# Kernel optimization log

Measured on AMD Instinct MI355X. Metric: run time of the kernel, lower is better.

## Reference

```python
import jax, jax.numpy as jnp
import numpy as np

B, S, D = 2, 2048, 4096
N_HEADS, N_KV_HEADS, HEAD_DIM = 32, 8, 128
Q_DIM = N_HEADS * HEAD_DIM        # 4096
KV_DIM = N_KV_HEADS * HEAD_DIM    # 1024
N_REP = N_HEADS // N_KV_HEADS
ROPE_THETA = 500000.0


def make_freqs_cis(seqlen, head_dim, theta):
    # Interleaved (sin, cos) pairs per rotary frequency, matching the module's
    # einsum/flip RoPE convention: row1 = x0*sin + x1*cos, row0 = x0*cos - x1*sin.
    inv_freq = 1.0 / (theta ** (np.arange(0, head_dim, 2, dtype=np.float32) / head_dim))
    t = np.arange(seqlen, dtype=np.float32)
    ang = np.outer(t, inv_freq)                       # [S, hd/2]
    fc = np.stack([np.sin(ang), np.cos(ang)], axis=-1)  # [S, hd/2, 2]
    return jnp.asarray(fc.reshape(seqlen, head_dim))


def apply_rotary_emb(xq, xk, freqs_cis):
    # xq: [B,S,Hq,hd], xk: [B,S,Hkv,hd], freqs_cis: [S,hd]
    xq_shape, xk_shape = xq.shape, xk.shape
    xq2 = xq.reshape(*xq.shape[:-1], -1, 2)
    xk2 = xk.reshape(*xk.shape[:-1], -1, 2)
    fc = freqs_cis.reshape(freqs_cis.shape[0], 1, -1, 2)   # [S,1,hd/2,2]
    # row_1 = <x, fc>
    xq_row1 = jnp.einsum('bshpi,shpi->bshp', xq2, fc)
    xk_row1 = jnp.einsum('bshpi,shpi->bshp', xk2, fc)
    # flipped fc with negated second component: (f1, -f0)
    fc_flip = jnp.flip(fc, axis=-1) * jnp.array([1.0, -1.0], dtype=fc.dtype)
    xq_row0 = jnp.einsum('bshpi,shpi->bshp', xq2, fc_flip)
    xk_row0 = jnp.einsum('bshpi,shpi->bshp', xk2, fc_flip)
    xq_out = jnp.stack([xq_row0, xq_row1], axis=-1).reshape(xq_shape)
    xk_out = jnp.stack([xk_row0, xk_row1], axis=-1).reshape(xk_shape)
    return xq_out, xk_out


def setup_inputs() -> dict:
    key = jax.random.key(0)
    k1, k2, k3 = jax.random.split(key, 3)
    x = jax.random.normal(k1, (B, S, D), dtype=jnp.float32)
    wqkv = jax.random.normal(k2, (D, Q_DIM + 2 * KV_DIM), dtype=jnp.float32) * 0.02
    wo = jax.random.normal(k3, (Q_DIM, D), dtype=jnp.float32) * 0.02
    freqs_cis = make_freqs_cis(S, HEAD_DIM, ROPE_THETA)
    return {"x": x, "freqs_cis": freqs_cis, "wqkv": wqkv, "wo": wo, "is_causal": 1}


def reference(x, freqs_cis, wqkv, wo, is_causal):
    bsz, seqlen, _ = x.shape
    xqkv = jnp.einsum('bsd,de->bse', x, wqkv)
    xq = xqkv[..., :Q_DIM].reshape(bsz, seqlen, N_HEADS, HEAD_DIM)
    xk = xqkv[..., Q_DIM:Q_DIM + KV_DIM].reshape(bsz, seqlen, N_KV_HEADS, HEAD_DIM)
    xv = xqkv[..., Q_DIM + KV_DIM:].reshape(bsz, seqlen, N_KV_HEADS, HEAD_DIM)
    xq, xk = apply_rotary_emb(xq, xk, freqs_cis)
    # [B,H,S,hd]
    xq = xq.transpose(0, 2, 1, 3)
    xk = jnp.repeat(xk.transpose(0, 2, 1, 3), N_REP, axis=1)
    xv = jnp.repeat(xv.transpose(0, 2, 1, 3), N_REP, axis=1)
    scale = 1.0 / jnp.sqrt(jnp.asarray(HEAD_DIM, dtype=xq.dtype))
    scores = jnp.einsum('bhqd,bhkd->bhqk', xq, xk) * scale
    if is_causal:
        mask = jnp.tril(jnp.ones((seqlen, seqlen), dtype=bool))
        scores = jnp.where(mask, scores, jnp.finfo(scores.dtype).min)
    attn = jax.nn.softmax(scores, axis=-1)
    out = jnp.einsum('bhqk,bhkd->bhqd', attn, xv)
    out = out.transpose(0, 2, 1, 3).reshape(bsz, seqlen, Q_DIM)
    return jnp.einsum('bsd,de->bse', out, wo)
```

## Files before the change

kernel.cpp:

```cpp
#include <hip/hip_runtime.h>
#include <stdint.h>
#include <stddef.h>

#define BB 2
#define SS 2048
#define DD 4096
#define NH 32
#define NKV 8
#define HD 128
#define QDIM 4096
#define KVDIM 1024
#define NQKV 6144
#define QK_SCALE_L2E 0.12751744f

typedef __bf16 bf16;
typedef __bf16 bf16x8 __attribute__((ext_vector_type(8)));
typedef __bf16 bf16x4 __attribute__((ext_vector_type(4)));
typedef float f32x4 __attribute__((ext_vector_type(4)));

#define MFMA16(a, b, c) __builtin_amdgcn_mfma_f32_16x16x32_bf16((a), (b), (c), 0, 0, 0)

typedef __attribute__((address_space(1))) void GASV;
typedef __attribute__((address_space(3))) void LASV;

__device__ __forceinline__ void gload_lds16(const void* g, void* l) {
    __builtin_amdgcn_global_load_lds((GASV*)g, (LASV*)l, 16, 0, 0);
}

__device__ __forceinline__ float fexp2(float x) {
    float r;
    asm("v_exp_f32 %0, %1" : "=v"(r) : "v"(x));
    return r;
}

__global__ __launch_bounds__(256) void k_cvt_x(const float* __restrict__ in,
                                               bf16* __restrict__ out) {
    size_t i = ((size_t)blockIdx.x * 256 + threadIdx.x) * 8;
    const float4 a = *(const float4*)(in + i);
    const float4 b = *(const float4*)(in + i + 4);
    bf16x8 v;
    v[0] = (bf16)a.x; v[1] = (bf16)a.y; v[2] = (bf16)a.z; v[3] = (bf16)a.w;
    v[4] = (bf16)b.x; v[5] = (bf16)b.y; v[6] = (bf16)b.z; v[7] = (bf16)b.w;
    *(bf16x8*)(out + i) = v;
}

__global__ __launch_bounds__(256) void k_tr_cvt(const float* __restrict__ in,
                                                bf16* __restrict__ out, int R, int C) {
    __shared__ float tile[64][65];
    const int t = threadIdx.x;
    const int tx = t & 15, ty = t >> 4;
    const int r0 = blockIdx.y * 64, c0 = blockIdx.x * 64;
#pragma unroll
    for (int p = 0; p < 4; ++p) {
        const float4 v = *(const float4*)(in + (size_t)(r0 + p * 16 + ty) * C + c0 + tx * 4);
        tile[p * 16 + ty][tx * 4 + 0] = v.x;
        tile[p * 16 + ty][tx * 4 + 1] = v.y;
        tile[p * 16 + ty][tx * 4 + 2] = v.z;
        tile[p * 16 + ty][tx * 4 + 3] = v.w;
    }
    __syncthreads();
#pragma unroll
    for (int p = 0; p < 4; ++p) {
        const int oc = c0 + p * 16 + ty;
        bf16x4 pk;
#pragma unroll
        for (int j = 0; j < 4; ++j) pk[j] = (bf16)tile[tx * 4 + j][p * 16 + ty];
        *(bf16x4*)(out + (size_t)oc * R + r0 + tx * 4) = pk;
    }
}

__device__ __forceinline__ void stage_tile64(bf16* lds, const bf16* gbase, int ld, int kt) {
    const int tid = threadIdx.x;
    const int lane = tid & 63;
    const int w = tid >> 6;
#pragma unroll
    for (int i = 0; i < 4; ++i) {
        const int phys = i * 4096 + w * 1024 + lane * 16;
        const int row = phys >> 7;
        const int cc = (phys >> 4) & 7;
        const int lc = cc ^ (row & 7);
        gload_lds16(gbase + (size_t)row * ld + kt + lc * 8,
                    (char*)lds + (i * 4096 + w * 1024));
    }
}

__device__ __forceinline__ void gemm_main(const bf16* __restrict__ Atile,
                                          const bf16* __restrict__ Btile,
                                          bf16* As, bf16* Bs, f32x4 acc[4][4]) {
    const int tid = threadIdx.x, lane = tid & 63, w = tid >> 6;
    const int wm = (w >> 1) * 64, wn = (w & 1) * 64;
    const int l15 = lane & 15, l4 = lane >> 4;
    const f32x4 vz = {0.f, 0.f, 0.f, 0.f};
#pragma unroll
    for (int m = 0; m < 4; ++m)
#pragma unroll
        for (int n = 0; n < 4; ++n) acc[m][n] = vz;

    for (int kt = 0; kt < 4096; kt += 64) {
        __syncthreads();
        stage_tile64(As, Atile, 4096, kt);
        stage_tile64(Bs, Btile, 4096, kt);
        __syncthreads();
#pragma unroll
        for (int kc = 0; kc < 2; ++kc) {
            bf16x8 af[4], bfr[4];
#pragma unroll
            for (int m = 0; m < 4; ++m) {
                const int row = wm + m * 16 + l15;
                const int cc = kc * 4 + l4;
                af[m] = *(const bf16x8*)((const char*)As + (row << 7) + ((cc ^ (row & 7)) << 4));
            }
#pragma unroll
            for (int n = 0; n < 4; ++n) {
                const int row = wn + n * 16 + l15;
                const int cc = kc * 4 + l4;
                bfr[n] = *(const bf16x8*)((const char*)Bs + (row << 7) + ((cc ^ (row & 7)) << 4));
            }
#pragma unroll
            for (int m = 0; m < 4; ++m)
#pragma unroll
                for (int n = 0; n < 4; ++n) acc[m][n] = MFMA16(af[m], bfr[n], acc[m][n]);
        }
    }
}

__global__ __launch_bounds__(256) void k_gemm_qkv(const bf16* __restrict__ A,
                                                  const bf16* __restrict__ Bt,
                                                  const float* __restrict__ fc,
                                                  bf16* __restrict__ Qb,
                                                  bf16* __restrict__ Kb,
                                                  bf16* __restrict__ VTb) {
    __shared__ __align__(16) bf16 As[128 * 64];
    __shared__ __align__(16) bf16 Bs[128 * 64];
    f32x4 acc[4][4];
    const int bx = blockIdx.x, by = blockIdx.y;
    gemm_main(A + (size_t)by * 128 * 4096, Bt + (size_t)bx * 128 * 4096, As, Bs, acc);

    const int tid = threadIdx.x, lane = tid & 63, w = tid >> 6;
    const int wm = (w >> 1) * 64, wn = (w & 1) * 64, l15 = lane & 15, l4 = lane >> 4;
    const int n0 = bx * 128 + wn;
#pragma unroll
    for (int m = 0; m < 4; ++m) {
        const int rowbase = by * 128 + wm + m * 16 + l4 * 4;
#pragma unroll
        for (int n = 0; n < 4; ++n) {
            const int col = n0 + n * 16 + l15;
            f32x4 v = acc[m][n];
            if (n0 < QDIM + KVDIM) {
                const int d = col & (HD - 1);
                const int dp = d & ~1;
                const float sgn = (d & 1) ? 1.f : -1.f;
#pragma unroll
                for (int r = 0; r < 4; ++r) {
                    const int row = rowbase + r;
                    const int s = row & (SS - 1);
                    const float2 sc = *(const float2*)(fc + s * HD + dp);
                    const float partner = __shfl_xor(v[r], 1);
                    float res = v[r] * sc.y + sgn * partner * sc.x;
                    if (n0 < QDIM) {
                        res *= QK_SCALE_L2E;
                        Qb[(size_t)row * QDIM + col] = (bf16)res;
                    } else {
                        Kb[(size_t)row * KVDIM + (col - QDIM)] = (bf16)res;
                    }
                }
            } else {
                const int hdv = col - (QDIM + KVDIM);
                const int kvh = hdv >> 7, dd = hdv & (HD - 1);
                const int bb = rowbase >> 11, s = rowbase & (SS - 1);
                bf16x4 pk;
#pragma unroll
                for (int r = 0; r < 4; ++r) pk[r] = (bf16)v[r];
                *(bf16x4*)(VTb + ((size_t)((bb * NKV + kvh) * HD + dd)) * SS + s) = pk;
            }
        }
    }
}

__global__ __launch_bounds__(256, 2) void k_attn(const bf16* __restrict__ Qb,
                                                 const bf16* __restrict__ Kb,
                                                 const bf16* __restrict__ VTb,
                                                 bf16* __restrict__ Ob) {
    __shared__ __align__(16) bf16 Ks[64 * 128];
    __shared__ __align__(16) bf16 Vs[128 * 64];
    __shared__ __align__(16) bf16 Ps[4][32 * 88];
    const int jj = blockIdx.x, h = blockIdx.y, b = blockIdx.z;
    const int kvh = h >> 2;
    const int tid = threadIdx.x, lane = tid & 63, w = tid >> 6;
    const int l15 = lane & 15, l4 = lane >> 4;

    const bf16* Kg = Kb + (size_t)b * SS * KVDIM + kvh * HD;
    const bf16* Vg = VTb + (size_t)(b * NKV + kvh) * HD * SS;

    int4 kreg[4], vreg[4];
    const f32x4 vz = {0.f, 0.f, 0.f, 0.f};

    auto issue_kv = [&](int t) {
#pragma unroll
        for (int i = 0; i < 4; ++i) {
            const int off = i * 4096 + tid * 16;
            const int row = off >> 8;
            const int cc = (off >> 4) & 15;
            kreg[i] = *(const int4*)((const char*)(Kg + (size_t)(t * 64 + row) * KVDIM) + cc * 16);
        }
#pragma unroll
        for (int i = 0; i < 4; ++i) {
            const int off = i * 4096 + tid * 16;
            const int row = off >> 7;
            const int cc = (off >> 4) & 7;
            vreg[i] = *(const int4*)((const char*)(Vg + (size_t)row * SS + t * 64) + cc * 16);
        }
    };

#pragma unroll 1
    for (int pj = 0; pj < 2; ++pj) {
        const int j = pj ? (15 - jj) : jj;
        const int q0 = j * 128;
        const int nt = 2 * j + 2;

        bf16x8 qf[2][4];
#pragma unroll
        for (int m = 0; m < 2; ++m) {
            const int qrow = q0 + w * 32 + m * 16 + l15;
            const bf16* qb = Qb + ((size_t)(b * SS + qrow) << 12) + h * HD + l4 * 8;
#pragma unroll
            for (int kc = 0; kc < 4; ++kc) qf[m][kc] = *(const bf16x8*)(qb + kc * 32);
        }

        f32x4 o[2][8];
#pragma unroll
        for (int m = 0; m < 2; ++m)
#pragma unroll
            for (int df = 0; df < 8; ++df) o[m][df] = vz;
        float m_run[2][4], l_run[2][4];
#pragma unroll
        for (int m = 0; m < 2; ++m)
#pragma unroll
            for (int r = 0; r < 4; ++r) { m_run[m][r] = -1e30f; l_run[m][r] = 0.f; }

        issue_kv(0);

        for (int t = 0; t < nt; ++t) {
            __syncthreads();
#pragma unroll
            for (int i = 0; i < 4; ++i) {
                const int off = i * 4096 + tid * 16;
                const int row = off >> 8;
                const int cc = (off >> 4) & 15;
                const int lc = cc ^ (row & 7);
                *(int4*)((char*)Ks + row * 256 + lc * 16) = kreg[i];
            }
#pragma unroll
            for (int i = 0; i < 4; ++i) {
                const int off = i * 4096 + tid * 16;
                const int row = off >> 7;
                const int cc = (off >> 4) & 7;
                const int lc = cc ^ (row & 7);
                *(int4*)((char*)Vs + row * 128 + lc * 16) = vreg[i];
            }
            __syncthreads();

            if (t + 1 < nt) issue_kv(t + 1);

            f32x4 sa[2][4];
#pragma unroll
            for (int m = 0; m < 2; ++m)
#pragma unroll
                for (int n = 0; n < 4; ++n) sa[m][n] = vz;
            __builtin_amdgcn_s_setprio(1);
#pragma unroll
            for (int kc = 0; kc < 4; ++kc)
#pragma unroll
                for (int n = 0; n < 4; ++n) {
                    const int krow = n * 16 + l15;
                    const int cc = kc * 4 + l4;
                    const bf16x8 kf =
                        *(const bf16x8*)((const char*)Ks + (krow << 8) + ((cc ^ (krow & 7)) << 4));
                    sa[0][n] = MFMA16(qf[0][kc], kf, sa[0][n]);
                    sa[1][n] = MFMA16(qf[1][kc], kf, sa[1][n]);
                }
            __builtin_amdgcn_s_setprio(0);

            if (t >= 2 * j) {
#pragma unroll
                for (int m = 0; m < 2; ++m)
#pragma unroll
                    for (int n = 0; n < 4; ++n)
#pragma unroll
                        for (int r = 0; r < 4; ++r) {
                            const int col = t * 64 + n * 16 + l15;
                            const int qr = q0 + w * 32 + m * 16 + l4 * 4 + r;
                            if (col > qr) sa[m][n][r] = -1e30f;
                        }
            }

#pragma unroll
            for (int m = 0; m < 2; ++m)
#pragma unroll
                for (int r = 0; r < 4; ++r) {
                    float mx = fmaxf(fmaxf(sa[m][0][r], sa[m][1][r]),
                                     fmaxf(sa[m][2][r], sa[m][3][r]));
#pragma unroll
                    for (int mk = 1; mk <= 8; mk <<= 1) mx = fmaxf(mx, __shfl_xor(mx, mk));
                    const float mn = fmaxf(m_run[m][r], mx);
                    const float alpha = fexp2(m_run[m][r] - mn);
                    m_run[m][r] = mn;
                    float rs = 0.f;
#pragma unroll
                    for (int n = 0; n < 4; ++n) {
                        const float p = fexp2(sa[m][n][r] - mn);
                        sa[m][n][r] = p;
                        rs += p;
                    }
#pragma unroll
                    for (int mk = 1; mk <= 8; mk <<= 1) rs += __shfl_xor(rs, mk);
                    l_run[m][r] = l_run[m][r] * alpha + rs;
#pragma unroll
                    for (int df = 0; df < 8; ++df) o[m][df][r] *= alpha;
                }

#pragma unroll
            for (int m = 0; m < 2; ++m)
#pragma unroll
                for (int n = 0; n < 4; ++n)
#pragma unroll
                    for (int r = 0; r < 4; ++r)
                        Ps[w][(m * 16 + l4 * 4 + r) * 88 + n * 16 + l15] = (bf16)sa[m][n][r];

            bf16x8 pf0[2], pf1[2];
#pragma unroll
            for (int ks = 0; ks < 2; ++ks) {
                pf0[ks] = *(const bf16x8*)(&Ps[w][l15 * 88 + ks * 32 + l4 * 8]);
                pf1[ks] = *(const bf16x8*)(&Ps[w][(16 + l15) * 88 + ks * 32 + l4 * 8]);
            }

            __builtin_amdgcn_s_setprio(1);
#pragma unroll
            for (int df = 0; df < 8; ++df)
#pragma unroll
                for (int ks = 0; ks < 2; ++ks) {
                    const int vrow = df * 16 + l15;
                    const int cc = ks * 4 + l4;
                    const bf16x8 vf =
                        *(const bf16x8*)((const char*)Vs + (vrow << 7) + ((cc ^ (vrow & 7)) << 4));
                    o[0][df] = MFMA16(pf0[ks], vf, o[0][df]);
                    o[1][df] = MFMA16(pf1[ks], vf, o[1][df]);
                }
            __builtin_amdgcn_s_setprio(0);
        }

#pragma unroll
        for (int m = 0; m < 2; ++m)
#pragma unroll
            for (int r = 0; r < 4; ++r) {
                const float inv = 1.f / l_run[m][r];
                const size_t row = (size_t)(b * SS + q0 + w * 32 + m * 16 + l4 * 4 + r);
#pragma unroll
                for (int df = 0; df < 8; ++df)
                    Ob[(row << 12) + h * HD + df * 16 + l15] = (bf16)(o[m][df][r] * inv);
            }
    }
}

__global__ __launch_bounds__(256) void k_gemm_out(const bf16* __restrict__ A,
                                                  const bf16* __restrict__ Bt,
                                                  float* __restrict__ out) {
    __shared__ __align__(16) bf16 As[128 * 64];
    __shared__ __align__(16) bf16 Bs[128 * 64];
    f32x4 acc[4][4];
    const int bx = blockIdx.x, by = blockIdx.y;
    gemm_main(A + (size_t)by * 128 * 4096, Bt + (size_t)bx * 128 * 4096, As, Bs, acc);

    const int tid = threadIdx.x, lane = tid & 63, w = tid >> 6;
    const int wm = (w >> 1) * 64, wn = (w & 1) * 64, l15 = lane & 15, l4 = lane >> 4;
#pragma unroll
    for (int m = 0; m < 4; ++m) {
        const int row = by * 128 + wm + m * 16 + l4 * 4;
#pragma unroll
        for (int n = 0; n < 4; ++n) {
            const int col = bx * 128 + wn + n * 16 + l15;
#pragma unroll
            for (int r = 0; r < 4; ++r) out[(size_t)(row + r) * DD + col] = acc[m][n][r];
        }
    }
}

extern "C" void kernel_launch(void* const* d_in, const int* in_sizes, int n_in,
                              void* d_out, int out_size, void* d_ws, size_t ws_size,
                              hipStream_t stream) {
    const float* x    = (const float*)d_in[0];
    const float* fc   = (const float*)d_in[1];
    const float* wqkv = (const float*)d_in[2];
    const float* wo   = (const float*)d_in[3];

    char* wsp = (char*)d_ws;
    const size_t MB = (size_t)1 << 20;
    bf16* xb    = (bf16*)(wsp);
    bf16* wqkvT = (bf16*)(wsp + 32 * MB);
    bf16* woT   = (bf16*)(wsp + 32 * MB);
    bf16* Qb    = (bf16*)(wsp + 80 * MB);
    bf16* Kb    = (bf16*)(wsp + 112 * MB);
    bf16* VTb   = (bf16*)(wsp + 120 * MB);
    bf16* Ab    = (bf16*)(wsp);
    float* out  = (float*)d_out;

    k_cvt_x<<<8192, 256, 0, stream>>>(x, xb);
    k_tr_cvt<<<dim3(NQKV / 64, DD / 64), 256, 0, stream>>>(wqkv, wqkvT, DD, NQKV);
    k_gemm_qkv<<<dim3(NQKV / 128, (BB * SS) / 128), 256, 0, stream>>>(xb, wqkvT, fc, Qb, Kb, VTb);
    k_tr_cvt<<<dim3(DD / 64, QDIM / 64), 256, 0, stream>>>(wo, woT, QDIM, DD);
    k_attn<<<dim3(8, NH, BB), 256, 0, stream>>>(Qb, Kb, VTb, Ab);
    k_gemm_out<<<dim3(DD / 128, (BB * SS) / 128), 256, 0, stream>>>(Ab, woT, out);
}
```

Before: 662.5 us.

## Replace GEMM core with 256x256 tile, 8-wave double-buffered pipelined mainloop

Both projection GEMMs now use 256x256 output tiles computed by 512 threads (8 waves). The K loop uses double-buffered LDS staging with async global-to-LDS loads issued two tiles ahead, partial vmcnt waits, and register-fragment prefetch interleaved with MFMA quadrants. The goal is to hide global-load latency and raise arithmetic intensity compared with the old 128x128 single-buffer loop, which synchronised twice per k-step. The cost is 128KB of LDS per block, heavy register pressure from 32 accumulators, and fewer blocks in the grid.

```diff
diff --git a/kernel.cpp b/kernel.cpp
--- a/kernel.cpp
+++ b/kernel.cpp
@@ -11,6 +11,7 @@
 #define QDIM 4096
 #define KVDIM 1024
 #define NQKV 6144
+#define NTILES 64
 #define QK_SCALE_L2E 0.12751744f
 
 typedef __bf16 bf16;
@@ -19,6 +20,8 @@
 typedef float f32x4 __attribute__((ext_vector_type(4)));
 
 #define MFMA16(a, b, c) __builtin_amdgcn_mfma_f32_16x16x32_bf16((a), (b), (c), 0, 0, 0)
+#define BAR() __builtin_amdgcn_s_barrier()
+#define VMW10() asm volatile("s_waitcnt vmcnt(10)" ::: "memory")
 
 typedef __attribute__((address_space(1))) void GASV;
 typedef __attribute__((address_space(3))) void LASV;
@@ -69,84 +72,149 @@
     }
 }
 
-__device__ __forceinline__ void stage_tile64(bf16* lds, const bf16* gbase, int ld, int kt) {
-    const int tid = threadIdx.x;
-    const int lane = tid & 63;
-    const int w = tid >> 6;
-#pragma unroll
-    for (int i = 0; i < 4; ++i) {
-        const int phys = i * 4096 + w * 1024 + lane * 16;
-        const int row = phys >> 7;
-        const int cc = (phys >> 4) & 7;
-        const int lc = cc ^ (row & 7);
-        gload_lds16(gbase + (size_t)row * ld + kt + lc * 8,
-                    (char*)lds + (i * 4096 + w * 1024));
-    }
-}
-
-__device__ __forceinline__ void gemm_main(const bf16* __restrict__ Atile,
-                                          const bf16* __restrict__ Btile,
-                                          bf16* As, bf16* Bs, f32x4 acc[4][4]) {
-    const int tid = threadIdx.x, lane = tid & 63, w = tid >> 6;
-    const int wm = (w >> 1) * 64, wn = (w & 1) * 64;
+
+__device__ __forceinline__ void stage_half(char* ldsRegion, const bf16* gsrc) {
+    const int t = threadIdx.x;
+    const int wid = t >> 6;
+#pragma unroll
+    for (int i = 0; i < 2; ++i) {
+        const int off = i * 8192 + t * 16;
+        const int row = off >> 7;
+        const int pc = (off >> 4) & 7;
+        const int lc = pc ^ (row & 7);
+        gload_lds16(gsrc + (size_t)row * 4096 + lc * 8,
+                    ldsRegion + i * 8192 + wid * 1024);
+    }
+}
+
+__device__ __forceinline__ void gemm256(const bf16* __restrict__ At,
+                                        const bf16* __restrict__ Bt,
+                                        char* LB, f32x4 acc[8][4]) {
+    const int tid = threadIdx.x, lane = tid & 63, wid = tid >> 6;
+    const int wm = wid >> 2, wn = wid & 3;
     const int l15 = lane & 15, l4 = lane >> 4;
+
     const f32x4 vz = {0.f, 0.f, 0.f, 0.f};
 #pragma unroll
-    for (int m = 0; m < 4; ++m)
+    for (int m = 0; m < 8; ++m)
 #pragma unroll
         for (int n = 0; n < 4; ++n) acc[m][n] = vz;
 
-    for (int kt = 0; kt < 4096; kt += 64) {
-        __syncthreads();
-        stage_tile64(As, Atile, 4096, kt);
-        stage_tile64(Bs, Btile, 4096, kt);
-        __syncthreads();
-#pragma unroll
-        for (int kc = 0; kc < 2; ++kc) {
-            bf16x8 af[4], bfr[4];
-#pragma unroll
-            for (int m = 0; m < 4; ++m) {
-                const int row = wm + m * 16 + l15;
-                const int cc = kc * 4 + l4;
-                af[m] = *(const bf16x8*)((const char*)As + (row << 7) + ((cc ^ (row & 7)) << 4));
-            }
-#pragma unroll
-            for (int n = 0; n < 4; ++n) {
-                const int row = wn + n * 16 + l15;
-                const int cc = kc * 4 + l4;
-                bfr[n] = *(const bf16x8*)((const char*)Bs + (row << 7) + ((cc ^ (row & 7)) << 4));
-            }
-#pragma unroll
-            for (int m = 0; m < 4; ++m)
-#pragma unroll
-                for (int n = 0; n < 4; ++n) acc[m][n] = MFMA16(af[m], bfr[n], acc[m][n]);
-        }
-    }
-}
-
-__global__ __launch_bounds__(256) void k_gemm_qkv(const bf16* __restrict__ A,
-                                                  const bf16* __restrict__ Bt,
-                                                  const float* __restrict__ fc,
-                                                  bf16* __restrict__ Qb,
-                                                  bf16* __restrict__ Kb,
-                                                  bf16* __restrict__ VTb) {
-    __shared__ __align__(16) bf16 As[128 * 64];
-    __shared__ __align__(16) bf16 Bs[128 * 64];
-    f32x4 acc[4][4];
+    auto Areg = [&](int db, int h) -> char* { return LB + db * 32768 + h * 16384; };
+    auto Breg = [&](int db, int h) -> char* { return LB + 65536 + db * 32768 + h * 16384; };
+
+    bf16x8 Aa[2][4], Ab[2][4], B0r[2][2], B1r[2][2];
+
+    auto loadA = [&](bf16x8 dst[2][4], int db, int h) {
+        char* base = Areg(db, h);
+#pragma unroll
+        for (int kk = 0; kk < 2; ++kk)
+#pragma unroll
+            for (int mf = 0; mf < 4; ++mf) {
+                const int row = wm * 64 + mf * 16 + l15;
+                const int cc = kk * 4 + l4;
+                dst[kk][mf] = *(const bf16x8*)(base + row * 128 + ((cc ^ (row & 7)) << 4));
+            }
+    };
+    auto loadB = [&](bf16x8 dst[2][2], int db, int h) {
+        char* base = Breg(db, h);
+#pragma unroll
+        for (int kk = 0; kk < 2; ++kk)
+#pragma unroll
+            for (int nf = 0; nf < 2; ++nf) {
+                const int row = wn * 32 + nf * 16 + l15;
+                const int cc = kk * 4 + l4;
+                dst[kk][nf] = *(const bf16x8*)(base + row * 128 + ((cc ^ (row & 7)) << 4));
+            }
+    };
+    auto stA = [&](int tau, int h) {
+        stage_half(Areg(tau & 1, h), At + (size_t)(h * 128) * 4096 + tau * 64);
+    };
+    auto stB = [&](int tau, int h) {
+        stage_half(Breg(tau & 1, h), Bt + (size_t)(h * 128) * 4096 + tau * 64);
+    };
+    auto mma = [&](bf16x8 A[2][4], bf16x8 B[2][2], int mb, int nb) {
+        __builtin_amdgcn_s_setprio(1);
+#pragma unroll
+        for (int kk = 0; kk < 2; ++kk)
+#pragma unroll
+            for (int mf = 0; mf < 4; ++mf)
+#pragma unroll
+                for (int nf = 0; nf < 2; ++nf)
+                    acc[mb + mf][nb + nf] = MFMA16(A[kk][mf], B[kk][nf], acc[mb + mf][nb + nf]);
+        __builtin_amdgcn_s_setprio(0);
+    };
+
+    stA(0, 0); stB(0, 0); stB(0, 1); stA(0, 1);
+    stA(1, 0); stB(1, 0); stB(1, 1); stA(1, 1);
+    asm volatile("s_waitcnt vmcnt(8)" ::: "memory");
+    BAR();
+    loadA(Aa, 0, 0);
+    loadB(B0r, 0, 0);
+
+#pragma unroll 1
+    for (int tau = 0; tau < NTILES - 2; ++tau) {
+        const int db = tau & 1, ndb = db ^ 1;
+        loadB(B1r, db, 1);
+        stA(tau + 2, 0);
+        VMW10(); BAR();
+        mma(Aa, B0r, 0, 0);
+        BAR();
+        loadA(Ab, db, 1);
+        stB(tau + 2, 0);
+        VMW10(); BAR();
+        mma(Aa, B1r, 0, 2);
+        BAR();
+        stB(tau + 2, 1);
+        VMW10(); BAR();
+        mma(Ab, B0r, 4, 0);
+        BAR();
+        loadA(Aa, ndb, 0);
+        loadB(B0r, ndb, 0);
+        stA(tau + 2, 1);
+        VMW10(); BAR();
+        mma(Ab, B1r, 4, 2);
+        BAR();
+    }
+
+    asm volatile("s_waitcnt vmcnt(0)" ::: "memory");
+    BAR();
+#pragma unroll 1
+    for (int tau = NTILES - 2; tau < NTILES; ++tau) {
+        const int db = tau & 1, ndb = db ^ 1;
+        loadB(B1r, db, 1);
+        BAR(); mma(Aa, B0r, 0, 0); BAR();
+        loadA(Ab, db, 1);
+        BAR(); mma(Aa, B1r, 0, 2); BAR();
+        BAR(); mma(Ab, B0r, 4, 0); BAR();
+        if (tau < NTILES - 1) { loadA(Aa, ndb, 0); loadB(B0r, ndb, 0); }
+        BAR(); mma(Ab, B1r, 4, 2); BAR();
+    }
+}
+
+__global__ __launch_bounds__(512, 2) void k_gemm_qkv(const bf16* __restrict__ A,
+                                                     const bf16* __restrict__ Bt,
+                                                     const float* __restrict__ fc,
+                                                     bf16* __restrict__ Qb,
+                                                     bf16* __restrict__ Kb,
+                                                     bf16* __restrict__ VTb) {
+    __shared__ __align__(16) char LB[131072];
+    f32x4 acc[8][4];
     const int bx = blockIdx.x, by = blockIdx.y;
-    gemm_main(A + (size_t)by * 128 * 4096, Bt + (size_t)bx * 128 * 4096, As, Bs, acc);
-
-    const int tid = threadIdx.x, lane = tid & 63, w = tid >> 6;
-    const int wm = (w >> 1) * 64, wn = (w & 1) * 64, l15 = lane & 15, l4 = lane >> 4;
-    const int n0 = bx * 128 + wn;
-#pragma unroll
-    for (int m = 0; m < 4; ++m) {
-        const int rowbase = by * 128 + wm + m * 16 + l4 * 4;
-#pragma unroll
-        for (int n = 0; n < 4; ++n) {
-            const int col = n0 + n * 16 + l15;
-            f32x4 v = acc[m][n];
-            if (n0 < QDIM + KVDIM) {
+    gemm256(A + (size_t)by * 256 * 4096, Bt + (size_t)bx * 256 * 4096, LB, acc);
+
+    const int tid = threadIdx.x, lane = tid & 63, wid = tid >> 6;
+    const int wm = wid >> 2, wn = wid & 3;
+    const int l15 = lane & 15, l4 = lane >> 4;
+    const int n0r = bx * 256;
+#pragma unroll
+    for (int mf = 0; mf < 8; ++mf) {
+        const int rowbase = by * 256 + (mf >> 2) * 128 + wm * 64 + (mf & 3) * 16 + l4 * 4;
+#pragma unroll
+        for (int nf = 0; nf < 4; ++nf) {
+            const int col = n0r + (nf >> 1) * 128 + wn * 32 + (nf & 1) * 16 + l15;
+            f32x4 v = acc[mf][nf];
+            if (n0r < QDIM + KVDIM) {
                 const int d = col & (HD - 1);
                 const int dp = d & ~1;
                 const float sgn = (d & 1) ? 1.f : -1.f;
@@ -157,7 +225,7 @@
                     const float2 sc = *(const float2*)(fc + s * HD + dp);
                     const float partner = __shfl_xor(v[r], 1);
                     float res = v[r] * sc.y + sgn * partner * sc.x;
-                    if (n0 < QDIM) {
+                    if (n0r < QDIM) {
                         res *= QK_SCALE_L2E;
                         Qb[(size_t)row * QDIM + col] = (bf16)res;
                     } else {
@@ -177,6 +245,29 @@
     }
 }
 
+__global__ __launch_bounds__(512, 2) void k_gemm_out(const bf16* __restrict__ A,
+                                                     const bf16* __restrict__ Bt,
+                                                     float* __restrict__ out) {
+    __shared__ __align__(16) char LB[131072];
+    f32x4 acc[8][4];
+    const int bx = blockIdx.x, by = blockIdx.y;
+    gemm256(A + (size_t)by * 256 * 4096, Bt + (size_t)bx * 256 * 4096, LB, acc);
+
+    const int tid = threadIdx.x, lane = tid & 63, wid = tid >> 6;
+    const int wm = wid >> 2, wn = wid & 3;
+    const int l15 = lane & 15, l4 = lane >> 4;
+#pragma unroll
+    for (int mf = 0; mf < 8; ++mf) {
+        const int row = by * 256 + (mf >> 2) * 128 + wm * 64 + (mf & 3) * 16 + l4 * 4;
+#pragma unroll
+        for (int nf = 0; nf < 4; ++nf) {
+            const int col = bx * 256 + (nf >> 1) * 128 + wn * 32 + (nf & 1) * 16 + l15;
+#pragma unroll
+            for (int r = 0; r < 4; ++r) out[(size_t)(row + r) * DD + col] = acc[mf][nf][r];
+        }
+    }
+}
+
 __global__ __launch_bounds__(256, 2) void k_attn(const bf16* __restrict__ Qb,
                                                  const bf16* __restrict__ Kb,
                                                  const bf16* __restrict__ VTb,
@@ -362,29 +453,6 @@
     }
 }
 
-__global__ __launch_bounds__(256) void k_gemm_out(const bf16* __restrict__ A,
-                                                  const bf16* __restrict__ Bt,
-                                                  float* __restrict__ out) {
-    __shared__ __align__(16) bf16 As[128 * 64];
-    __shared__ __align__(16) bf16 Bs[128 * 64];
-    f32x4 acc[4][4];
-    const int bx = blockIdx.x, by = blockIdx.y;
-    gemm_main(A + (size_t)by * 128 * 4096, Bt + (size_t)bx * 128 * 4096, As, Bs, acc);
-
-    const int tid = threadIdx.x, lane = tid & 63, w = tid >> 6;
-    const int wm = (w >> 1) * 64, wn = (w & 1) * 64, l15 = lane & 15, l4 = lane >> 4;
-#pragma unroll
-    for (int m = 0; m < 4; ++m) {
-        const int row = by * 128 + wm + m * 16 + l4 * 4;
-#pragma unroll
-        for (int n = 0; n < 4; ++n) {
-            const int col = bx * 128 + wn + n * 16 + l15;
-#pragma unroll
-            for (int r = 0; r < 4; ++r) out[(size_t)(row + r) * DD + col] = acc[m][n][r];
-        }
-    }
-}
-
 extern "C" void kernel_launch(void* const* d_in, const int* in_sizes, int n_in,
                               void* d_out, int out_size, void* d_ws, size_t ws_size,
                               hipStream_t stream) {
@@ -406,8 +474,8 @@
 
     k_cvt_x<<<8192, 256, 0, stream>>>(x, xb);
     k_tr_cvt<<<dim3(NQKV / 64, DD / 64), 256, 0, stream>>>(wqkv, wqkvT, DD, NQKV);
-    k_gemm_qkv<<<dim3(NQKV / 128, (BB * SS) / 128), 256, 0, stream>>>(xb, wqkvT, fc, Qb, Kb, VTb);
+    k_gemm_qkv<<<dim3(NQKV / 256, (BB * SS) / 256), 512, 0, stream>>>(xb, wqkvT, fc, Qb, Kb, VTb);
     k_tr_cvt<<<dim3(DD / 64, QDIM / 64), 256, 0, stream>>>(wo, woT, QDIM, DD);
     k_attn<<<dim3(8, NH, BB), 256, 0, stream>>>(Qb, Kb, VTb, Ab);
-    k_gemm_out<<<dim3(DD / 128, (BB * SS) / 128), 256, 0, stream>>>(Ab, woT, out);
-}
+    k_gemm_out<<<dim3(DD / 256, (BB * SS) / 256), 512, 0, stream>>>(Ab, woT, out);
+}
```

New measurement: 608.8 us. 1.09x faster.
